# Optimization experiments

Measured on AMD Instinct MI355X. Metric: run time of the kernel, lower is better.

Reference implementation:

```python
import jax, jax.numpy as jnp
import numpy as np

N_EMBD = 1024
HEAD_SIZE = 64
B, T = 8, 4096


def setup_inputs() -> dict:
    key = jax.random.key(0)
    kx, kk, kq, kv = jax.random.split(key, 4)
    scale = 1.0 / np.sqrt(N_EMBD)
    x = jax.random.normal(kx, (B, T, N_EMBD), dtype=jnp.float32)
    # nn.Linear(N_EMBD, head_size, bias=False) weights, stored as [in, out] for x @ W
    W_k = jax.random.uniform(kk, (N_EMBD, HEAD_SIZE), dtype=jnp.float32, minval=-scale, maxval=scale)
    W_q = jax.random.uniform(kq, (N_EMBD, HEAD_SIZE), dtype=jnp.float32, minval=-scale, maxval=scale)
    W_v = jax.random.uniform(kv, (N_EMBD, HEAD_SIZE), dtype=jnp.float32, minval=-scale, maxval=scale)
    return {"x": x, "W_k": W_k, "W_q": W_q, "W_v": W_v}


def reference(x, W_k, W_q, W_v) -> jnp.ndarray:
    # x: [B,T,E]; projections to [B,T,H]
    k = jnp.einsum("bte,eh->bth", x, W_k)
    q = jnp.einsum("bte,eh->bth", x, W_q)
    v = jnp.einsum("bte,eh->bth", x, W_v)
    H = W_k.shape[1]
    scores = jnp.einsum("bth,bsh->bts", q, k) * (H ** -0.5)  # [B,T,T]
    Tlen = x.shape[1]
    causal = jnp.tril(jnp.ones((Tlen, Tlen), dtype=bool))
    scores = jnp.where(causal, scores, -jnp.inf)
    attn = jax.nn.softmax(scores, axis=-1)
    # dropout is identity in eval mode (deterministic reference)
    return jnp.einsum("bts,bsh->bth", attn, v)
```

## Files before the change

### kernel.cpp

```cpp
#include <hip/hip_runtime.h>
#include <hip/hip_bf16.h>


#define BB 8
#define TT 4096
#define EE 1024
#define HH 64

typedef __attribute__((ext_vector_type(8))) short short8;
typedef __attribute__((ext_vector_type(4))) float floatx4;
typedef short8 __attribute__((may_alias)) short8_a;
typedef uint2 __attribute__((may_alias)) uint2_a;
typedef uint4 __attribute__((may_alias)) uint4_a;
typedef float4 __attribute__((may_alias)) float4_a;

#define GLDS(gp, lp)                                                     \
  __builtin_amdgcn_global_load_lds(                                      \
      (const __attribute__((address_space(1))) unsigned int*)(gp),       \
      (__attribute__((address_space(3))) unsigned int*)(lp), 16, 0, 0)

__device__ __forceinline__ unsigned short f2bf(float f) {
  union { float f; unsigned int u; } v; v.f = f;
  unsigned int r = v.u + 0x7fffu + ((v.u >> 16) & 1u);
  return (unsigned short)(r >> 16);
}
__device__ __forceinline__ unsigned int pk2(float a, float b) {
  return (unsigned int)f2bf(a) | ((unsigned int)f2bf(b) << 16);
}
__device__ __forceinline__ floatx4 fzero() {
  floatx4 z = {0.f, 0.f, 0.f, 0.f};
  return z;
}
__device__ __forceinline__ floatx4 mfma_bf16(short8 a, short8 b, floatx4 c) {
  return __builtin_amdgcn_mfma_f32_16x16x32_bf16(a, b, c, 0, 0, 0);
}
__device__ __forceinline__ short8 pack8(float4 a, float4 b) {
  union { unsigned int u[4]; short8 s; } r;
  r.u[0] = pk2(a.x, a.y);
  r.u[1] = pk2(a.z, a.w);
  r.u[2] = pk2(b.x, b.y);
  r.u[3] = pk2(b.z, b.w);
  return r.s;
}

__global__ __launch_bounds__(256) void wt_kernel(
    const float* __restrict__ Wk, const float* __restrict__ Wq,
    const float* __restrict__ Wv, unsigned short* __restrict__ wt3) {
  __shared__ float tile[64][65];
  const int m = blockIdx.y;
  const int eb = blockIdx.x;
  const float* W = (m == 0) ? Wk : ((m == 1) ? Wq : Wv);
  const int t = threadIdx.x;
  {
    const int r = t >> 2;
    const int c0 = (t & 3) * 16;
    const float* src = W + (size_t)(eb * 64 + r) * 64 + c0;
#pragma unroll
    for (int i = 0; i < 16; ++i) tile[r][c0 + i] = src[i];
  }
  __syncthreads();
  {
    const int h = t >> 2;
    const int e0 = (t & 3) * 16;
    unsigned int w[8];
#pragma unroll
    for (int i = 0; i < 8; ++i)
      w[i] = pk2(tile[e0 + 2 * i][h], tile[e0 + 2 * i + 1][h]);
    unsigned short* dst = wt3 + (size_t)(m * 64 + h) * EE + eb * 64 + e0;
    ((uint4_a*)dst)[0] = make_uint4(w[0], w[1], w[2], w[3]);
    ((uint4_a*)(dst + 8))[0] = make_uint4(w[4], w[5], w[6], w[7]);
  }
}

__global__ __launch_bounds__(256) void proj_kernel(
    const float* __restrict__ x, const unsigned short* __restrict__ wt3,
    unsigned short* __restrict__ kws, unsigned short* __restrict__ qws,
    unsigned short* __restrict__ vtws) {
  __shared__ unsigned short Bl[2][24][512];
  const int t = threadIdx.x;
  const int wv = t >> 6, lane = t & 63;
  const int l16 = lane & 15, quad = lane >> 4;
  const int mshalf = wv & 1;
  const int jbase = (wv >> 1) * 6;
  const size_t row0 = (size_t)blockIdx.x * 64;

  floatx4 acc[6][2];
#pragma unroll
  for (int j = 0; j < 6; ++j)
#pragma unroll
    for (int m2 = 0; m2 < 2; ++m2) acc[j][m2] = fzero();

  const float* xbase = x + (row0 + mshalf * 32 + l16) * EE + quad * 8;

  float4 ra[2][2][2], rb[2][2][2];
#pragma unroll
  for (int m2 = 0; m2 < 2; ++m2)
#pragma unroll
    for (int f = 0; f < 2; ++f)
#pragma unroll
      for (int g = 0; g < 2; ++g)
        ra[m2][f][g] = *(const float4_a*)(xbase + (size_t)m2 * 16 * EE + f * 32 + g * 4);

#define STAGE_B(buf, kc)                                                       \
  {                                                                            \
    _Pragma("unroll") for (int i = 0; i < 6; ++i) {                            \
      const int idx = wv * 6 + i;                                              \
      const int j = idx >> 1, f = idx & 1;                                     \
      const unsigned short* gp =                                               \
          wt3 + (size_t)(j * 16 + l16) * EE + (kc) + f * 32 + quad * 8;        \
      GLDS(gp, &Bl[buf][idx][0]);                                              \
    }                                                                          \
  }

  STAGE_B(0, 0);
  __syncthreads();

  for (int c = 0; c < 16; ++c) {
    const int cur = c & 1;
    if (c < 15) {
      STAGE_B(cur ^ 1, (c + 1) * 64);
#pragma unroll
      for (int m2 = 0; m2 < 2; ++m2)
#pragma unroll
        for (int f = 0; f < 2; ++f)
#pragma unroll
          for (int g = 0; g < 2; ++g)
            rb[m2][f][g] = *(const float4_a*)(xbase + (size_t)m2 * 16 * EE +
                                              (c + 1) * 64 + f * 32 + g * 4);
    }
    short8 af[2][2];
#pragma unroll
    for (int m2 = 0; m2 < 2; ++m2)
#pragma unroll
      for (int f = 0; f < 2; ++f) af[m2][f] = pack8(ra[m2][f][0], ra[m2][f][1]);
#pragma unroll
    for (int j = 0; j < 6; ++j)
#pragma unroll
      for (int f = 0; f < 2; ++f) {
        short8 bf = *(const short8_a*)&Bl[cur][(jbase + j) * 2 + f][lane * 8];
#pragma unroll
        for (int m2 = 0; m2 < 2; ++m2)
          acc[j][m2] = mfma_bf16(af[m2][f], bf, acc[j][m2]);
      }
#pragma unroll
    for (int m2 = 0; m2 < 2; ++m2)
#pragma unroll
      for (int f = 0; f < 2; ++f)
#pragma unroll
        for (int g = 0; g < 2; ++g) ra[m2][f][g] = rb[m2][f][g];
    __syncthreads();
  }
#undef STAGE_B

  const int b = (int)(row0 >> 12);
  const int tt0 = (int)(row0 & (TT - 1));
#pragma unroll
  for (int j = 0; j < 6; ++j) {
    const int jg = jbase + j;
    const int m = jg >> 2;
    const int h0 = (jg & 3) * 16;
#pragma unroll
    for (int m2 = 0; m2 < 2; ++m2) {
      floatx4 a = acc[j][m2];
      const int rbase = mshalf * 32 + m2 * 16 + quad * 4;
      if (m == 0) {
#pragma unroll
        for (int r = 0; r < 4; ++r)
          kws[(row0 + rbase + r) * HH + h0 + l16] = f2bf(a[r]);
      } else if (m == 1) {
#pragma unroll
        for (int r = 0; r < 4; ++r)
          qws[(row0 + rbase + r) * HH + h0 + l16] = f2bf(a[r] * 0.125f);
      } else {
        uint2 p;
        p.x = pk2(a[0], a[1]);
        p.y = pk2(a[2], a[3]);
        ((uint2_a*)&vtws[(size_t)(b * 64 + h0 + l16) * TT + tt0 + rbase])[0] = p;
      }
    }
  }
}

__global__ __launch_bounds__(256) void attn_kernel(
    const unsigned short* __restrict__ kws, const unsigned short* __restrict__ qws,
    const unsigned short* __restrict__ vtws, float* __restrict__ out) {
  __shared__ unsigned short KV[2][16][512];
  __shared__ unsigned short pb[4][16][72];
  const int t = threadIdx.x;
  const int wv = t >> 6, lane = t & 63;
  const int l16 = lane & 15, quad = lane >> 4;
  const int id = (int)blockIdx.x;
  const int r255 = id & 255;
  const int b = r255 & 7;
  const int m = r255 >> 3;
  const int jq = (id < 256) ? m : 63 - m;
  const int q0 = jq * 64;
  const int dt = jq;
  const int qrow = q0 + wv * 16 + l16;

  const unsigned short* qp = qws + ((size_t)b * TT + qrow) * HH + quad * 8;
  short8 qa0 = *(const short8_a*)(qp);
  short8 qa1 = *(const short8_a*)(qp + 32);

  floatx4 o[4];
#pragma unroll
  for (int nt = 0; nt < 4; ++nt) o[nt] = fzero();
  float lsum = 0.f;

#define STAGE_KV(buf, ks)                                                      \
  {                                                                            \
    _Pragma("unroll") for (int i = 0; i < 4; ++i) {                            \
      const int idx = wv * 4 + i;                                              \
      const unsigned short* gp;                                                \
      if (idx < 8) {                                                           \
        const int nt = idx >> 1, f = idx & 1;                                  \
        gp = kws + ((size_t)b * TT + (ks) + nt * 16 + l16) * HH + f * 32 +     \
             quad * 8;                                                         \
      } else {                                                                 \
        const int nt = (idx - 8) >> 1, f = idx & 1;                            \
        gp = vtws + ((size_t)(b * 64 + nt * 16 + l16)) * TT + (ks) + f * 32 +  \
             quad * 8;                                                         \
      }                                                                        \
      GLDS(gp, &KV[buf][idx][0]);                                              \
    }                                                                          \
  }

  STAGE_KV(0, 0);
  __syncthreads();

  for (int kt = 0; kt <= dt; ++kt) {
    const int cur = kt & 1;
    const int ks = kt * 64;
    if (kt < dt) STAGE_KV(cur ^ 1, ks + 64);

    floatx4 s[4];
#pragma unroll
    for (int nt = 0; nt < 4; ++nt) {
      short8 kf0 = *(const short8_a*)&KV[cur][nt * 2][lane * 8];
      short8 kf1 = *(const short8_a*)&KV[cur][nt * 2 + 1][lane * 8];
      floatx4 z = fzero();
      z = mfma_bf16(kf0, qa0, z);
      z = mfma_bf16(kf1, qa1, z);
      s[nt] = z;
    }
    if (kt == dt) {
#pragma unroll
      for (int nt = 0; nt < 4; ++nt)
#pragma unroll
        for (int r = 0; r < 4; ++r) {
          const int key = ks + nt * 16 + quad * 4 + r;
          if (key > qrow) s[nt][r] = -1e30f;
        }
    }
#pragma unroll
    for (int nt = 0; nt < 4; ++nt) {
      const float p0 = __expf(s[nt][0]);
      const float p1 = __expf(s[nt][1]);
      const float p2 = __expf(s[nt][2]);
      const float p3 = __expf(s[nt][3]);
      lsum += (p0 + p1) + (p2 + p3);
      uint2 pw;
      pw.x = pk2(p0, p1);
      pw.y = pk2(p2, p3);
      ((uint2_a*)&pb[wv][l16][nt * 16 + quad * 4])[0] = pw;
    }
    short8 pf0 = *(const short8_a*)&pb[wv][l16][quad * 8];
    short8 pf1 = *(const short8_a*)&pb[wv][l16][quad * 8 + 32];
#pragma unroll
    for (int nt = 0; nt < 4; ++nt) {
      short8 vf0 = *(const short8_a*)&KV[cur][8 + nt * 2][lane * 8];
      short8 vf1 = *(const short8_a*)&KV[cur][8 + nt * 2 + 1][lane * 8];
      o[nt] = mfma_bf16(vf0, pf0, o[nt]);
      o[nt] = mfma_bf16(vf1, pf1, o[nt]);
    }
    __syncthreads();
  }
#undef STAGE_KV

  float lr = lsum;
  lr += __shfl_xor(lr, 16);
  lr += __shfl_xor(lr, 32);
  const float inv = 1.0f / lr;
#pragma unroll
  for (int nt = 0; nt < 4; ++nt) {
    float4 st;
    st.x = o[nt][0] * inv;
    st.y = o[nt][1] * inv;
    st.z = o[nt][2] * inv;
    st.w = o[nt][3] * inv;
    *(float4_a*)&out[((size_t)b * TT + qrow) * HH + nt * 16 + quad * 4] = st;
  }
}

extern "C" void kernel_launch(void* const* d_in, const int* in_sizes, int n_in,
                              void* d_out, int out_size, void* d_ws, size_t ws_size,
                              hipStream_t stream) {
  const float* x = (const float*)d_in[0];
  const float* Wk = (const float*)d_in[1];
  const float* Wq = (const float*)d_in[2];
  const float* Wv = (const float*)d_in[3];
  float* out = (float*)d_out;

  unsigned short* kws = (unsigned short*)d_ws;
  unsigned short* qws = kws + (size_t)BB * TT * HH;
  unsigned short* vtws = qws + (size_t)BB * TT * HH;
  unsigned short* wt3 = vtws + (size_t)BB * TT * HH;

  hipLaunchKernelGGL(wt_kernel, dim3(16, 3), dim3(256), 0, stream, Wk, Wq, Wv, wt3);
  hipLaunchKernelGGL(proj_kernel, dim3(512), dim3(256), 0, stream, x, wt3, kws, qws,
                     vtws);
  hipLaunchKernelGGL(attn_kernel, dim3(512), dim3(256), 0, stream, kws, qws,
                     vtws, out);
}
```

Measured before the change: 303.9 us.

## Split attention over key chunks with combine pass and shrink projection tiles

The projection kernel moves to 32-row blocks (1024 blocks) and reads weights straight from global memory instead of staging them through LDS. The attention kernel splits each query block's causal key range into chunks of 16 tiles, giving 1280 blocks. Each block writes an unnormalized partial output and row sum, and a new combine kernel adds the partials and normalizes. This targets load imbalance and low occupancy from long causal rows, at the cost of extra global traffic for the partials, an extra launch, and dropping the KV double buffer in favour of sync, load, sync.

```diff
diff --git a/kernel.cpp b/kernel.cpp
--- a/kernel.cpp
+++ b/kernel.cpp
@@ -6,6 +6,7 @@
 #define TT 4096
 #define EE 1024
 #define HH 64
+#define BT (BB * TT)
 
 typedef __attribute__((ext_vector_type(8))) short short8;
 typedef __attribute__((ext_vector_type(4))) float floatx4;
@@ -76,93 +77,74 @@
     const float* __restrict__ x, const unsigned short* __restrict__ wt3,
     unsigned short* __restrict__ kws, unsigned short* __restrict__ qws,
     unsigned short* __restrict__ vtws) {
-  __shared__ unsigned short Bl[2][24][512];
   const int t = threadIdx.x;
   const int wv = t >> 6, lane = t & 63;
   const int l16 = lane & 15, quad = lane >> 4;
-  const int mshalf = wv & 1;
-  const int jbase = (wv >> 1) * 6;
-  const size_t row0 = (size_t)blockIdx.x * 64;
-
-  floatx4 acc[6][2];
-#pragma unroll
-  for (int j = 0; j < 6; ++j)
+  const size_t row0 = (size_t)blockIdx.x * 32;
+
+  floatx4 acc[3][2];
+#pragma unroll
+  for (int j = 0; j < 3; ++j)
 #pragma unroll
     for (int m2 = 0; m2 < 2; ++m2) acc[j][m2] = fzero();
 
-  const float* xbase = x + (row0 + mshalf * 32 + l16) * EE + quad * 8;
-
-  float4 ra[2][2][2], rb[2][2][2];
+  const float* xb = x + (row0 + l16) * EE + quad * 8;
+
+  float4 buf[2][2][2][2];
 #pragma unroll
   for (int m2 = 0; m2 < 2; ++m2)
 #pragma unroll
     for (int f = 0; f < 2; ++f)
 #pragma unroll
       for (int g = 0; g < 2; ++g)
-        ra[m2][f][g] = *(const float4_a*)(xbase + (size_t)m2 * 16 * EE + f * 32 + g * 4);
-
-#define STAGE_B(buf, kc)                                                       \
-  {                                                                            \
-    _Pragma("unroll") for (int i = 0; i < 6; ++i) {                            \
-      const int idx = wv * 6 + i;                                              \
-      const int j = idx >> 1, f = idx & 1;                                     \
-      const unsigned short* gp =                                               \
-          wt3 + (size_t)(j * 16 + l16) * EE + (kc) + f * 32 + quad * 8;        \
-      GLDS(gp, &Bl[buf][idx][0]);                                              \
-    }                                                                          \
-  }
-
-  STAGE_B(0, 0);
-  __syncthreads();
+        buf[0][m2][f][g] =
+            *(const float4_a*)(xb + (size_t)m2 * 16 * EE + f * 32 + g * 4);
 
   for (int c = 0; c < 16; ++c) {
     const int cur = c & 1;
     if (c < 15) {
-      STAGE_B(cur ^ 1, (c + 1) * 64);
 #pragma unroll
       for (int m2 = 0; m2 < 2; ++m2)
 #pragma unroll
         for (int f = 0; f < 2; ++f)
 #pragma unroll
           for (int g = 0; g < 2; ++g)
-            rb[m2][f][g] = *(const float4_a*)(xbase + (size_t)m2 * 16 * EE +
-                                              (c + 1) * 64 + f * 32 + g * 4);
+            buf[cur ^ 1][m2][f][g] = *(const float4_a*)(
+                xb + (size_t)m2 * 16 * EE + (c + 1) * 64 + f * 32 + g * 4);
     }
     short8 af[2][2];
 #pragma unroll
     for (int m2 = 0; m2 < 2; ++m2)
 #pragma unroll
-      for (int f = 0; f < 2; ++f) af[m2][f] = pack8(ra[m2][f][0], ra[m2][f][1]);
-#pragma unroll
-    for (int j = 0; j < 6; ++j)
-#pragma unroll
-      for (int f = 0; f < 2; ++f) {
-        short8 bf = *(const short8_a*)&Bl[cur][(jbase + j) * 2 + f][lane * 8];
-#pragma unroll
-        for (int m2 = 0; m2 < 2; ++m2)
-          acc[j][m2] = mfma_bf16(af[m2][f], bf, acc[j][m2]);
+      for (int f = 0; f < 2; ++f)
+        af[m2][f] = pack8(buf[cur][m2][f][0], buf[cur][m2][f][1]);
+#pragma unroll
+    for (int j = 0; j < 3; ++j) {
+      const int jg = wv * 3 + j;
+      const unsigned short* wp =
+          wt3 + (size_t)((jg >> 2) * 64 + (jg & 3) * 16 + l16) * EE + c * 64 +
+          quad * 8;
+      short8 b0 = *(const short8_a*)(wp);
+      short8 b1 = *(const short8_a*)(wp + 32);
+#pragma unroll
+      for (int m2 = 0; m2 < 2; ++m2) {
+        acc[j][m2] = mfma_bf16(af[m2][0], b0, acc[j][m2]);
+        acc[j][m2] = mfma_bf16(af[m2][1], b1, acc[j][m2]);
       }
-#pragma unroll
-    for (int m2 = 0; m2 < 2; ++m2)
-#pragma unroll
-      for (int f = 0; f < 2; ++f)
-#pragma unroll
-        for (int g = 0; g < 2; ++g) ra[m2][f][g] = rb[m2][f][g];
-    __syncthreads();
-  }
-#undef STAGE_B
+    }
+  }
 
   const int b = (int)(row0 >> 12);
   const int tt0 = (int)(row0 & (TT - 1));
 #pragma unroll
-  for (int j = 0; j < 6; ++j) {
-    const int jg = jbase + j;
+  for (int j = 0; j < 3; ++j) {
+    const int jg = wv * 3 + j;
     const int m = jg >> 2;
     const int h0 = (jg & 3) * 16;
 #pragma unroll
     for (int m2 = 0; m2 < 2; ++m2) {
       floatx4 a = acc[j][m2];
-      const int rbase = mshalf * 32 + m2 * 16 + quad * 4;
+      const int rbase = m2 * 16 + quad * 4;
       if (m == 0) {
 #pragma unroll
         for (int r = 0; r < 4; ++r)
@@ -183,19 +165,28 @@
 
 __global__ __launch_bounds__(256) void attn_kernel(
     const unsigned short* __restrict__ kws, const unsigned short* __restrict__ qws,
-    const unsigned short* __restrict__ vtws, float* __restrict__ out) {
-  __shared__ unsigned short KV[2][16][512];
+    const unsigned short* __restrict__ vtws, float* __restrict__ o_part,
+    float* __restrict__ l_part) {
+  __shared__ unsigned short KV[16][512];
   __shared__ unsigned short pb[4][16][72];
   const int t = threadIdx.x;
   const int wv = t >> 6, lane = t & 63;
   const int l16 = lane & 15, quad = lane >> 4;
-  const int id = (int)blockIdx.x;
-  const int r255 = id & 255;
-  const int b = r255 & 7;
-  const int m = r255 >> 3;
-  const int jq = (id < 256) ? m : 63 - m;
+  const int g = (int)blockIdx.x;
+  const int b = g & 7;
+  const int i = g >> 3;
+  int s, jq;
+  if (i < 49)       { s = 0; jq = 15 + i; }
+  else if (i < 82)  { s = 1; jq = 31 + (i - 49); }
+  else if (i < 99)  { s = 2; jq = 47 + (i - 82); }
+  else if (i == 99) { s = 3; jq = 63; }
+  else if (i < 115) { s = 0; jq = 114 - i; }
+  else if (i < 130) { s = 1; jq = 16 + (129 - i); }
+  else if (i < 145) { s = 2; jq = 32 + (144 - i); }
+  else              { s = 3; jq = 48 + (159 - i); }
+  const int k0 = s * 16;
+  const int nit = min(16, jq + 1 - k0);
   const int q0 = jq * 64;
-  const int dt = jq;
   const int qrow = q0 + wv * 16 + l16;
 
   const unsigned short* qp = qws + ((size_t)b * TT + qrow) * HH + quad * 8;
@@ -207,57 +198,56 @@
   for (int nt = 0; nt < 4; ++nt) o[nt] = fzero();
   float lsum = 0.f;
 
-#define STAGE_KV(buf, ks)                                                      \
-  {                                                                            \
-    _Pragma("unroll") for (int i = 0; i < 4; ++i) {                            \
-      const int idx = wv * 4 + i;                                              \
-      const unsigned short* gp;                                                \
-      if (idx < 8) {                                                           \
-        const int nt = idx >> 1, f = idx & 1;                                  \
-        gp = kws + ((size_t)b * TT + (ks) + nt * 16 + l16) * HH + f * 32 +     \
-             quad * 8;                                                         \
-      } else {                                                                 \
-        const int nt = (idx - 8) >> 1, f = idx & 1;                            \
-        gp = vtws + ((size_t)(b * 64 + nt * 16 + l16)) * TT + (ks) + f * 32 +  \
-             quad * 8;                                                         \
-      }                                                                        \
-      GLDS(gp, &KV[buf][idx][0]);                                              \
-    }                                                                          \
-  }
-
-  STAGE_KV(0, 0);
+#define STAGE_KV(ks)                                                          \
+  {                                                                           \
+    _Pragma("unroll") for (int ii = 0; ii < 4; ++ii) {                        \
+      const int idx = wv * 4 + ii;                                            \
+      const unsigned short* gp;                                               \
+      if (idx < 8) {                                                          \
+        const int nt = idx >> 1, f = idx & 1;                                 \
+        gp = kws + ((size_t)b * TT + (ks) + nt * 16 + l16) * HH + f * 32 +    \
+             quad * 8;                                                        \
+      } else {                                                                \
+        const int nt = (idx - 8) >> 1, f = idx & 1;                           \
+        gp = vtws + ((size_t)(b * 64 + nt * 16 + l16)) * TT + (ks) + f * 32 + \
+             quad * 8;                                                        \
+      }                                                                       \
+      GLDS(gp, &KV[idx][0]);                                                  \
+    }                                                                         \
+  }
+
+  STAGE_KV(k0 * 64);
   __syncthreads();
 
-  for (int kt = 0; kt <= dt; ++kt) {
-    const int cur = kt & 1;
+  for (int it = 0; it < nit; ++it) {
+    const int kt = k0 + it;
     const int ks = kt * 64;
-    if (kt < dt) STAGE_KV(cur ^ 1, ks + 64);
-
-    floatx4 s[4];
+
+    floatx4 sv[4];
 #pragma unroll
     for (int nt = 0; nt < 4; ++nt) {
-      short8 kf0 = *(const short8_a*)&KV[cur][nt * 2][lane * 8];
-      short8 kf1 = *(const short8_a*)&KV[cur][nt * 2 + 1][lane * 8];
+      short8 kf0 = *(const short8_a*)&KV[nt * 2][lane * 8];
+      short8 kf1 = *(const short8_a*)&KV[nt * 2 + 1][lane * 8];
       floatx4 z = fzero();
       z = mfma_bf16(kf0, qa0, z);
       z = mfma_bf16(kf1, qa1, z);
-      s[nt] = z;
-    }
-    if (kt == dt) {
+      sv[nt] = z;
+    }
+    if (kt == jq) {
 #pragma unroll
       for (int nt = 0; nt < 4; ++nt)
 #pragma unroll
         for (int r = 0; r < 4; ++r) {
           const int key = ks + nt * 16 + quad * 4 + r;
-          if (key > qrow) s[nt][r] = -1e30f;
+          if (key > qrow) sv[nt][r] = -1e30f;
         }
     }
 #pragma unroll
     for (int nt = 0; nt < 4; ++nt) {
-      const float p0 = __expf(s[nt][0]);
-      const float p1 = __expf(s[nt][1]);
-      const float p2 = __expf(s[nt][2]);
-      const float p3 = __expf(s[nt][3]);
+      const float p0 = __expf(sv[nt][0]);
+      const float p1 = __expf(sv[nt][1]);
+      const float p2 = __expf(sv[nt][2]);
+      const float p3 = __expf(sv[nt][3]);
       lsum += (p0 + p1) + (p2 + p3);
       uint2 pw;
       pw.x = pk2(p0, p1);
@@ -268,28 +258,60 @@
     short8 pf1 = *(const short8_a*)&pb[wv][l16][quad * 8 + 32];
 #pragma unroll
     for (int nt = 0; nt < 4; ++nt) {
-      short8 vf0 = *(const short8_a*)&KV[cur][8 + nt * 2][lane * 8];
-      short8 vf1 = *(const short8_a*)&KV[cur][8 + nt * 2 + 1][lane * 8];
+      short8 vf0 = *(const short8_a*)&KV[8 + nt * 2][lane * 8];
+      short8 vf1 = *(const short8_a*)&KV[8 + nt * 2 + 1][lane * 8];
       o[nt] = mfma_bf16(vf0, pf0, o[nt]);
       o[nt] = mfma_bf16(vf1, pf1, o[nt]);
     }
-    __syncthreads();
+    if (it + 1 < nit) {
+      __syncthreads();
+      STAGE_KV((kt + 1) * 64);
+      __syncthreads();
+    }
   }
 #undef STAGE_KV
 
   float lr = lsum;
   lr += __shfl_xor(lr, 16);
   lr += __shfl_xor(lr, 32);
-  const float inv = 1.0f / lr;
+  float* op = o_part + ((size_t)s * BT + (size_t)b * TT + qrow) * HH;
 #pragma unroll
   for (int nt = 0; nt < 4; ++nt) {
     float4 st;
-    st.x = o[nt][0] * inv;
-    st.y = o[nt][1] * inv;
-    st.z = o[nt][2] * inv;
-    st.w = o[nt][3] * inv;
-    *(float4_a*)&out[((size_t)b * TT + qrow) * HH + nt * 16 + quad * 4] = st;
-  }
+    st.x = o[nt][0];
+    st.y = o[nt][1];
+    st.z = o[nt][2];
+    st.w = o[nt][3];
+    *(float4_a*)(op + nt * 16 + quad * 4) = st;
+  }
+  if (quad == 0) l_part[(size_t)s * BT + (size_t)b * TT + qrow] = lr;
+}
+
+__global__ __launch_bounds__(256) void comb_kernel(
+    const float* __restrict__ o_part, const float* __restrict__ l_part,
+    float* __restrict__ out) {
+  const int g = (int)blockIdx.x * 256 + (int)threadIdx.x;
+  const int bt = g >> 3;
+  const int h0 = (g & 7) * 8;
+  const int tq = bt & (TT - 1);
+  const int nch = (tq >> 10) + 1;
+  float4 a0 = make_float4(0.f, 0.f, 0.f, 0.f);
+  float4 a1 = make_float4(0.f, 0.f, 0.f, 0.f);
+  float l = 0.f;
+  for (int s = 0; s < nch; ++s) {
+    const float* p = o_part + ((size_t)s * BT + bt) * HH + h0;
+    float4 x0 = *(const float4_a*)(p);
+    float4 x1 = *(const float4_a*)(p + 4);
+    a0.x += x0.x; a0.y += x0.y; a0.z += x0.z; a0.w += x0.w;
+    a1.x += x1.x; a1.y += x1.y; a1.z += x1.z; a1.w += x1.w;
+    l += l_part[(size_t)s * BT + bt];
+  }
+  const float inv = 1.0f / l;
+  a0.x *= inv; a0.y *= inv; a0.z *= inv; a0.w *= inv;
+  a1.x *= inv; a1.y *= inv; a1.z *= inv; a1.w *= inv;
+  float* op = out + (size_t)bt * HH + h0;
+  *(float4_a*)(op) = a0;
+  *(float4_a*)(op + 4) = a1;
 }
 
 extern "C" void kernel_launch(void* const* d_in, const int* in_sizes, int n_in,
@@ -302,13 +324,17 @@
   float* out = (float*)d_out;
 
   unsigned short* kws = (unsigned short*)d_ws;
-  unsigned short* qws = kws + (size_t)BB * TT * HH;
-  unsigned short* vtws = qws + (size_t)BB * TT * HH;
-  unsigned short* wt3 = vtws + (size_t)BB * TT * HH;
+  unsigned short* qws = kws + (size_t)BT * HH;
+  unsigned short* vtws = qws + (size_t)BT * HH;
+  unsigned short* wt3 = vtws + (size_t)BT * HH;
+  float* o_part = (float*)((char*)d_ws + 12976128);
+  float* l_part = (float*)((char*)d_ws + 46530560);
 
   hipLaunchKernelGGL(wt_kernel, dim3(16, 3), dim3(256), 0, stream, Wk, Wq, Wv, wt3);
-  hipLaunchKernelGGL(proj_kernel, dim3(512), dim3(256), 0, stream, x, wt3, kws, qws,
-                     vtws);
-  hipLaunchKernelGGL(attn_kernel, dim3(512), dim3(256), 0, stream, kws, qws,
-                     vtws, out);
-}
+  hipLaunchKernelGGL(proj_kernel, dim3(1024), dim3(256), 0, stream, x, wt3, kws,
+                     qws, vtws);
+  hipLaunchKernelGGL(attn_kernel, dim3(1280), dim3(256), 0, stream, kws, qws, vtws,
+                     o_part, l_part);
+  hipLaunchKernelGGL(comb_kernel, dim3(1024), dim3(256), 0, stream, o_part, l_part,
+                     out);
+}
```

Result: slower. 490.9 us (+61.5%).
